# Kernel tuning notes

Measured on AMD Instinct MI355X. Metric: run time of the kernel, lower is better.

## Reference

```python
import jax, jax.numpy as jnp
import numpy as np


def setup_inputs() -> dict:
    key = jax.random.key(0)
    ks = jax.random.split(key, 8)
    B, N, E, F = 8, 200, 128, 16
    scale = 0.05
    return {
        "h": jax.random.normal(ks[0], (B, N, E), dtype=jnp.float32),
        "edge_features": jax.random.normal(ks[1], (B, N, N, F), dtype=jnp.float32),
        "W": jax.random.uniform(ks[2], (B, N, N), dtype=jnp.float32),
        "W_node": jax.random.normal(ks[3], (E, E), dtype=jnp.float32) * scale,
        "W_edge": jax.random.normal(ks[4], (E, F), dtype=jnp.float32) * scale,
        "W_weight": jax.random.normal(ks[5], (E, 1), dtype=jnp.float32) * scale,
        "W_out": jax.random.normal(ks[6], (E, E), dtype=jnp.float32) * scale,
        "b_out": jax.random.normal(ks[7], (E,), dtype=jnp.float32) * scale,
    }


def reference(h, edge_features, W, W_node, W_edge, W_weight, W_out, b_out):
    # hi: [B,N,1,E]  (node_proj)
    hi = jnp.einsum('bne,fe->bnf', h, W_node)[:, :, None, :]
    # ej: [B,N,N,E]  (edge_proj)
    ej = jnp.einsum('bnmf,ef->bnme', edge_features, W_edge)
    # wij: [B,N,N,E] (weight_proj of scalar W)
    wij = W[..., None] * W_weight[:, 0]  # broadcast [B,N,N,1]*[E]
    msg = jnp.tanh(hi + ej + wij)        # [B,N,N,E]
    agg = msg.mean(axis=2)               # [B,N,E]
    return jnp.einsum('bne,fe->bnf', agg, W_out) + b_out
```

## Files before the change

### kernel.cpp

```cpp
#include <hip/hip_runtime.h>

typedef __attribute__((ext_vector_type(4))) float  f32x4;
typedef __attribute__((ext_vector_type(8))) short  short8;
typedef __attribute__((ext_vector_type(2))) unsigned int u32x2;

#define BN_TOTAL 1600
#define NN 200
#define EDIM 128
#define FDIM 16
#define AROW_STRIDE 40

__device__ __forceinline__ unsigned short f2bf(float f) {
    unsigned u = __float_as_uint(f);
    u += 0x7FFFu + ((u >> 16) & 1u);
    return (unsigned short)(u >> 16);
}

__device__ __forceinline__ float tanh_fast(float x) {
    float e = __builtin_amdgcn_exp2f(x * 2.8853900817779268f);
    float r = __builtin_amdgcn_rcpf(1.0f + e);
    return __builtin_fmaf(-2.0f, r, 1.0f);
}

__global__ __launch_bounds__(256) void rowproj_kernel(
    const float* __restrict__ in, const float* __restrict__ Wm,
    const float* __restrict__ bias, float* __restrict__ out, int has_bias)
{
    __shared__ float s[2048];
    const int tid  = threadIdx.x;
    const int row0 = blockIdx.x * 8;

    for (int idx = tid; idx < 1024; idx += 256) {
        int r = idx >> 7, e = idx & 127;
        s[e * 16 + r] = in[(row0 + r) * EDIM + e];
    }
    __syncthreads();

    const int f = tid & 127;
    const int c = tid >> 7;
    float acc[8];
#pragma unroll
    for (int r = 0; r < 8; ++r) acc[r] = 0.0f;

    const float* wrow = Wm + f * EDIM + c * 64;
    for (int j = 0; j < 64; j += 4) {
        f32x4 w4 = *(const f32x4*)(wrow + j);
#pragma unroll
        for (int jj = 0; jj < 4; ++jj) {
            int e = c * 64 + j + jj;
            float w = w4[jj];
            f32x4 a = *(const f32x4*)(s + e * 16);
            f32x4 b = *(const f32x4*)(s + e * 16 + 4);
            acc[0] = __builtin_fmaf(a.x, w, acc[0]);
            acc[1] = __builtin_fmaf(a.y, w, acc[1]);
            acc[2] = __builtin_fmaf(a.z, w, acc[2]);
            acc[3] = __builtin_fmaf(a.w, w, acc[3]);
            acc[4] = __builtin_fmaf(b.x, w, acc[4]);
            acc[5] = __builtin_fmaf(b.y, w, acc[5]);
            acc[6] = __builtin_fmaf(b.z, w, acc[6]);
            acc[7] = __builtin_fmaf(b.w, w, acc[7]);
        }
    }
    __syncthreads();
    {
        f32x4 lo = {acc[0], acc[1], acc[2], acc[3]};
        f32x4 hi = {acc[4], acc[5], acc[6], acc[7]};
        *(f32x4*)(s + (c * 128 + f) * 8)     = lo;
        *(f32x4*)(s + (c * 128 + f) * 8 + 4) = hi;
    }
    __syncthreads();
    if (tid < 128) {
        float bv = has_bias ? bias[tid] : 0.0f;
#pragma unroll
        for (int r = 0; r < 8; ++r) {
            float v = s[tid * 8 + r] + s[(128 + tid) * 8 + r] + bv;
            out[(row0 + r) * EDIM + tid] = v;
        }
    }
}

__global__ __launch_bounds__(512) void msg_kernel(
    const float* __restrict__ ef, const float* __restrict__ Wadj,
    const float* __restrict__ W_edge, const float* __restrict__ W_weight,
    float* __restrict__ hi_agg)
{
    __shared__ short Abf[208 * AROW_STRIDE];
    const int tid  = threadIdx.x;
    const int bn   = blockIdx.x;
    const int lane = tid & 63;
    const int wid  = tid >> 6;
    const int g    = lane >> 4;
    const int l15  = lane & 15;
    const int e_b  = wid * 16 + l15;

    float hi_e = hi_agg[bn * EDIM + e_b];

    short8 bfrag = {0, 0, 0, 0, 0, 0, 0, 0};
    if (g < 2) {
        const float* p = W_edge + e_b * FDIM + g * 8;
        f32x4 v0 = *(const f32x4*)(p);
        f32x4 v1 = *(const f32x4*)(p + 4);
        bfrag[0] = (short)f2bf(v0.x); bfrag[1] = (short)f2bf(v0.y);
        bfrag[2] = (short)f2bf(v0.z); bfrag[3] = (short)f2bf(v0.w);
        bfrag[4] = (short)f2bf(v1.x); bfrag[5] = (short)f2bf(v1.y);
        bfrag[6] = (short)f2bf(v1.z); bfrag[7] = (short)f2bf(v1.w);
    } else if (g == 2) {
        bfrag[0] = (short)f2bf(W_weight[e_b]);
    }

    {
        f32x4 z = {0.0f, 0.0f, 0.0f, 0.0f};
        for (int o = tid; o < 1040; o += 512)
            *(f32x4*)(Abf + o * 8) = z;
    }
    __syncthreads();

    for (int idx = tid; idx < 800; idx += 512) {
        int m  = idx >> 2;
        int k4 = (idx & 3) * 4;
        f32x4 v = *(const f32x4*)(ef + (size_t)bn * (NN * FDIM) + idx * 4);
        unsigned lo = (unsigned)f2bf(v.x) | ((unsigned)f2bf(v.y) << 16);
        unsigned hi = (unsigned)f2bf(v.z) | ((unsigned)f2bf(v.w) << 16);
        u32x2 pk = {lo, hi};
        *(u32x2*)(Abf + m * AROW_STRIDE + k4) = pk;
    }
    for (int m = tid; m < NN; m += 512)
        Abf[m * AROW_STRIDE + 16] = (short)f2bf(Wadj[bn * NN + m]);
    __syncthreads();

    const f32x4 zero4 = {0.0f, 0.0f, 0.0f, 0.0f};
    float part = 0.0f;
#pragma unroll
    for (int mt = 0; mt < 13; ++mt) {
        short8 a = *(const short8*)(Abf + (mt * 16 + l15) * AROW_STRIDE + g * 8);
        f32x4 cacc = __builtin_amdgcn_mfma_f32_16x16x32_bf16(a, bfrag, zero4, 0, 0, 0);
        if (mt < 12) {
            part += tanh_fast(cacc[0] + hi_e);
            part += tanh_fast(cacc[1] + hi_e);
            part += tanh_fast(cacc[2] + hi_e);
            part += tanh_fast(cacc[3] + hi_e);
        } else if (g < 2) {
            part += tanh_fast(cacc[0] + hi_e);
            part += tanh_fast(cacc[1] + hi_e);
            part += tanh_fast(cacc[2] + hi_e);
            part += tanh_fast(cacc[3] + hi_e);
        }
    }
    part += __shfl_xor(part, 16);
    part += __shfl_xor(part, 32);

    if (lane < 16)
        hi_agg[bn * EDIM + wid * 16 + lane] = part * (1.0f / 200.0f);
}

extern "C" void kernel_launch(void* const* d_in, const int* in_sizes, int n_in,
                              void* d_out, int out_size, void* d_ws, size_t ws_size,
                              hipStream_t stream) {
    const float* h        = (const float*)d_in[0];
    const float* ef       = (const float*)d_in[1];
    const float* W        = (const float*)d_in[2];
    const float* W_node   = (const float*)d_in[3];
    const float* W_edge   = (const float*)d_in[4];
    const float* W_weight = (const float*)d_in[5];
    const float* W_out    = (const float*)d_in[6];
    const float* b_out    = (const float*)d_in[7];
    float* out = (float*)d_out;

    rowproj_kernel<<<200, 256, 0, stream>>>(h, W_node, b_out, out, 0);
    msg_kernel<<<BN_TOTAL, 512, 0, stream>>>(ef, W, W_edge, W_weight, out);
    rowproj_kernel<<<200, 256, 0, stream>>>(out, W_out, b_out, out, 1);
}
```

Baseline: 30.25 us.

## Fuse node projection, message aggregation and output projection into one kernel

Replaces the three-kernel pipeline with a single per-row kernel. The node projection is computed with bf16 MFMA and fed in as the accumulator initializer of the message MFMA, which removes the separate hi add. The output projection is done in-block from LDS with a four-way reduction. This removes two launches and the global round trips of the intermediates. In exchange, each block redundantly reads a full W_node slice and all of W_out, and the node projection now runs in bf16 rather than fp32, which adds rounding error.

```diff
diff --git a/kernel.cpp b/kernel.cpp
--- a/kernel.cpp
+++ b/kernel.cpp
@@ -4,7 +4,6 @@
 typedef __attribute__((ext_vector_type(8))) short  short8;
 typedef __attribute__((ext_vector_type(2))) unsigned int u32x2;
 
-#define BN_TOTAL 1600
 #define NN 200
 #define EDIM 128
 #define FDIM 16
@@ -22,69 +21,17 @@
     return __builtin_fmaf(-2.0f, r, 1.0f);
 }
 
-__global__ __launch_bounds__(256) void rowproj_kernel(
-    const float* __restrict__ in, const float* __restrict__ Wm,
-    const float* __restrict__ bias, float* __restrict__ out, int has_bias)
-{
-    __shared__ float s[2048];
-    const int tid  = threadIdx.x;
-    const int row0 = blockIdx.x * 8;
-
-    for (int idx = tid; idx < 1024; idx += 256) {
-        int r = idx >> 7, e = idx & 127;
-        s[e * 16 + r] = in[(row0 + r) * EDIM + e];
-    }
-    __syncthreads();
-
-    const int f = tid & 127;
-    const int c = tid >> 7;
-    float acc[8];
-#pragma unroll
-    for (int r = 0; r < 8; ++r) acc[r] = 0.0f;
-
-    const float* wrow = Wm + f * EDIM + c * 64;
-    for (int j = 0; j < 64; j += 4) {
-        f32x4 w4 = *(const f32x4*)(wrow + j);
-#pragma unroll
-        for (int jj = 0; jj < 4; ++jj) {
-            int e = c * 64 + j + jj;
-            float w = w4[jj];
-            f32x4 a = *(const f32x4*)(s + e * 16);
-            f32x4 b = *(const f32x4*)(s + e * 16 + 4);
-            acc[0] = __builtin_fmaf(a.x, w, acc[0]);
-            acc[1] = __builtin_fmaf(a.y, w, acc[1]);
-            acc[2] = __builtin_fmaf(a.z, w, acc[2]);
-            acc[3] = __builtin_fmaf(a.w, w, acc[3]);
-            acc[4] = __builtin_fmaf(b.x, w, acc[4]);
-            acc[5] = __builtin_fmaf(b.y, w, acc[5]);
-            acc[6] = __builtin_fmaf(b.z, w, acc[6]);
-            acc[7] = __builtin_fmaf(b.w, w, acc[7]);
-        }
-    }
-    __syncthreads();
-    {
-        f32x4 lo = {acc[0], acc[1], acc[2], acc[3]};
-        f32x4 hi = {acc[4], acc[5], acc[6], acc[7]};
-        *(f32x4*)(s + (c * 128 + f) * 8)     = lo;
-        *(f32x4*)(s + (c * 128 + f) * 8 + 4) = hi;
-    }
-    __syncthreads();
-    if (tid < 128) {
-        float bv = has_bias ? bias[tid] : 0.0f;
-#pragma unroll
-        for (int r = 0; r < 8; ++r) {
-            float v = s[tid * 8 + r] + s[(128 + tid) * 8 + r] + bv;
-            out[(row0 + r) * EDIM + tid] = v;
-        }
-    }
-}
-
-__global__ __launch_bounds__(512) void msg_kernel(
-    const float* __restrict__ ef, const float* __restrict__ Wadj,
+__global__ __launch_bounds__(512) void fused_kernel(
+    const float* __restrict__ h, const float* __restrict__ ef,
+    const float* __restrict__ Wadj, const float* __restrict__ W_node,
     const float* __restrict__ W_edge, const float* __restrict__ W_weight,
-    float* __restrict__ hi_agg)
+    const float* __restrict__ W_out, const float* __restrict__ b_out,
+    float* __restrict__ out)
 {
     __shared__ short Abf[208 * AROW_STRIDE];
+    __shared__ float agg_lds[EDIM];
+    __shared__ float red[512];
+
     const int tid  = threadIdx.x;
     const int bn   = blockIdx.x;
     const int lane = tid & 63;
@@ -92,8 +39,6 @@
     const int g    = lane >> 4;
     const int l15  = lane & 15;
     const int e_b  = wid * 16 + l15;
-
-    float hi_e = hi_agg[bn * EDIM + e_b];
 
     short8 bfrag = {0, 0, 0, 0, 0, 0, 0, 0};
     if (g < 2) {
@@ -108,49 +53,100 @@
         bfrag[0] = (short)f2bf(W_weight[e_b]);
     }
 
+    short8 ah[4], bn4[4];
     {
-        f32x4 z = {0.0f, 0.0f, 0.0f, 0.0f};
-        for (int o = tid; o < 1040; o += 512)
-            *(f32x4*)(Abf + o * 8) = z;
+        const float* hrow = h + bn * EDIM;
+        const float* wrow = W_node + e_b * EDIM;
+#pragma unroll
+        for (int s = 0; s < 4; ++s) {
+            int k0 = s * 32 + g * 8;
+            f32x4 a0 = *(const f32x4*)(hrow + k0);
+            f32x4 a1 = *(const f32x4*)(hrow + k0 + 4);
+            f32x4 w0 = *(const f32x4*)(wrow + k0);
+            f32x4 w1 = *(const f32x4*)(wrow + k0 + 4);
+            short8 av, wv;
+            av[0]=(short)f2bf(a0.x); av[1]=(short)f2bf(a0.y);
+            av[2]=(short)f2bf(a0.z); av[3]=(short)f2bf(a0.w);
+            av[4]=(short)f2bf(a1.x); av[5]=(short)f2bf(a1.y);
+            av[6]=(short)f2bf(a1.z); av[7]=(short)f2bf(a1.w);
+            wv[0]=(short)f2bf(w0.x); wv[1]=(short)f2bf(w0.y);
+            wv[2]=(short)f2bf(w0.z); wv[3]=(short)f2bf(w0.w);
+            wv[4]=(short)f2bf(w1.x); wv[5]=(short)f2bf(w1.y);
+            wv[6]=(short)f2bf(w1.z); wv[7]=(short)f2bf(w1.w);
+            ah[s] = av; bn4[s] = wv;
+        }
     }
-    __syncthreads();
 
     for (int idx = tid; idx < 800; idx += 512) {
         int m  = idx >> 2;
         int k4 = (idx & 3) * 4;
         f32x4 v = *(const f32x4*)(ef + (size_t)bn * (NN * FDIM) + idx * 4);
         unsigned lo = (unsigned)f2bf(v.x) | ((unsigned)f2bf(v.y) << 16);
-        unsigned hi = (unsigned)f2bf(v.z) | ((unsigned)f2bf(v.w) << 16);
-        u32x2 pk = {lo, hi};
+        unsigned hi2 = (unsigned)f2bf(v.z) | ((unsigned)f2bf(v.w) << 16);
+        u32x2 pk = {lo, hi2};
         *(u32x2*)(Abf + m * AROW_STRIDE + k4) = pk;
     }
-    for (int m = tid; m < NN; m += 512)
-        Abf[m * AROW_STRIDE + 16] = (short)f2bf(Wadj[bn * NN + m]);
+    {
+        const short8 z = {0,0,0,0,0,0,0,0};
+        for (int m = tid; m < 208; m += 512) {
+            short wv = (m < NN) ? (short)f2bf(Wadj[bn * NN + m]) : (short)0;
+            short8 zw = {wv,0,0,0,0,0,0,0};
+            *(short8*)(Abf + m * AROW_STRIDE + 16) = zw;
+            *(short8*)(Abf + m * AROW_STRIDE + 24) = z;
+            if (m >= NN) {
+                *(short8*)(Abf + m * AROW_STRIDE)     = z;
+                *(short8*)(Abf + m * AROW_STRIDE + 8) = z;
+            }
+        }
+    }
+
+    f32x4 hiacc = {0.0f, 0.0f, 0.0f, 0.0f};
+#pragma unroll
+    for (int s = 0; s < 4; ++s)
+        hiacc = __builtin_amdgcn_mfma_f32_16x16x32_bf16(ah[s], bn4[s], hiacc, 0, 0, 0);
+
     __syncthreads();
 
-    const f32x4 zero4 = {0.0f, 0.0f, 0.0f, 0.0f};
     float part = 0.0f;
 #pragma unroll
     for (int mt = 0; mt < 13; ++mt) {
         short8 a = *(const short8*)(Abf + (mt * 16 + l15) * AROW_STRIDE + g * 8);
-        f32x4 cacc = __builtin_amdgcn_mfma_f32_16x16x32_bf16(a, bfrag, zero4, 0, 0, 0);
-        if (mt < 12) {
-            part += tanh_fast(cacc[0] + hi_e);
-            part += tanh_fast(cacc[1] + hi_e);
-            part += tanh_fast(cacc[2] + hi_e);
-            part += tanh_fast(cacc[3] + hi_e);
-        } else if (g < 2) {
-            part += tanh_fast(cacc[0] + hi_e);
-            part += tanh_fast(cacc[1] + hi_e);
-            part += tanh_fast(cacc[2] + hi_e);
-            part += tanh_fast(cacc[3] + hi_e);
+        f32x4 cacc = __builtin_amdgcn_mfma_f32_16x16x32_bf16(a, bfrag, hiacc, 0, 0, 0);
+        if (mt < 12 || g < 2) {
+            part += tanh_fast(cacc[0]);
+            part += tanh_fast(cacc[1]);
+            part += tanh_fast(cacc[2]);
+            part += tanh_fast(cacc[3]);
         }
     }
     part += __shfl_xor(part, 16);
     part += __shfl_xor(part, 32);
 
     if (lane < 16)
-        hi_agg[bn * EDIM + wid * 16 + lane] = part * (1.0f / 200.0f);
+        agg_lds[wid * 16 + lane] = part * (1.0f / 200.0f);
+    __syncthreads();
+
+    {
+        const int f = tid & 127;
+        const int c = tid >> 7;
+        const float* wrow = W_out + f * EDIM + c * 32;
+        const float* arow = agg_lds + c * 32;
+        float o = 0.0f;
+#pragma unroll
+        for (int j = 0; j < 32; j += 4) {
+            f32x4 w4 = *(const f32x4*)(wrow + j);
+            f32x4 a4 = *(const f32x4*)(arow + j);
+            o = __builtin_fmaf(w4.x, a4.x, o);
+            o = __builtin_fmaf(w4.y, a4.y, o);
+            o = __builtin_fmaf(w4.z, a4.z, o);
+            o = __builtin_fmaf(w4.w, a4.w, o);
+        }
+        red[tid] = o;
+    }
+    __syncthreads();
+    if (tid < 128)
+        out[bn * EDIM + tid] = red[tid] + red[tid + 128] + red[tid + 256]
+                             + red[tid + 384] + b_out[tid];
 }
 
 extern "C" void kernel_launch(void* const* d_in, const int* in_sizes, int n_in,
@@ -166,7 +162,6 @@
     const float* b_out    = (const float*)d_in[7];
     float* out = (float*)d_out;
 
-    rowproj_kernel<<<200, 256, 0, stream>>>(h, W_node, b_out, out, 0);
-    msg_kernel<<<BN_TOTAL, 512, 0, stream>>>(ef, W, W_edge, W_weight, out);
-    rowproj_kernel<<<200, 256, 0, stream>>>(out, W_out, b_out, out, 1);
+    fused_kernel<<<1600, 512, 0, stream>>>(h, ef, W, W_node, W_edge, W_weight,
+                                           W_out, b_out, out);
 }
```

After: 42.31 us. 39.8% more time.
